# Optimization experiments

Hardware: AMD Instinct MI355X
Metric: run time of the kernel (lower is better)

## Reference

```python
import jax, jax.numpy as jnp
import numpy as np

B, T, HID = 2, 2048, 1024
NH = 8
QK_DIM = 1024
V_DIM = 2048
SCALE_BASE = 512.0
GN_EPS = 1e-5


def _xpos_rotate(x, downscale):
    # x: [B, T, QK_DIM]; XPOS rotary embedding (syncdoth/RetNet, offset=0)
    d = QK_DIM
    dh = d // 2
    pos = jnp.arange(T, dtype=jnp.float32)
    # per-pair magnitude scale
    base_scale = (jnp.arange(0, d, 2, dtype=jnp.float32) + 0.4 * d) / (1.4 * d)  # [dh]
    scale = base_scale[None, :] ** (pos[:, None] / SCALE_BASE)  # [T, dh]
    if downscale:
        scale = 1.0 / scale
    inv_freq = 1.0 / (10000.0 ** (jnp.arange(dh, dtype=jnp.float32) / dh))
    sinusoid = pos[:, None] * inv_freq[None, :]  # [T, dh]
    sin = jnp.sin(sinusoid) * scale
    cos = jnp.cos(sinusoid) * scale
    # duplicate_interleave -> [T, d]
    sin = jnp.repeat(sin, 2, axis=-1)
    cos = jnp.repeat(cos, 2, axis=-1)
    x1 = x[..., 0::2]
    x2 = x[..., 1::2]
    rot = jnp.stack((-x2, x1), axis=-1).reshape(x.shape)  # rotate_every_two
    return x * cos[None] + rot * sin[None]


def setup_inputs() -> dict:
    key = jax.random.key(0)
    k1, k2, k3, k4 = jax.random.split(key, 4)
    x = jax.random.normal(k1, (B, T, HID), dtype=jnp.float32)
    Wqkv = jax.random.normal(k2, (HID, 2 * QK_DIM + V_DIM), dtype=jnp.float32) / np.sqrt(HID)
    Wg = jax.random.normal(k3, (HID, V_DIM), dtype=jnp.float32) / np.sqrt(HID)
    Wp = jax.random.normal(k4, (V_DIM, HID), dtype=jnp.float32) / np.sqrt(V_DIM)
    bp = jnp.zeros((HID,), dtype=jnp.float32)
    return {"x": x, "Wqkv": Wqkv, "Wg": Wg, "Wp": Wp, "bp": bp}


def reference(x, Wqkv, Wg, Wp, bp):
    # multi-scale decay (non-default gamma path)
    gamma = 1.0 - jnp.exp(jnp.linspace(np.log(1.0 / 32), np.log(1.0 / 512), NH)).astype(jnp.float32)  # [NH]

    qkv = x @ Wqkv  # [B,T,2qk+v]
    q, k, v = jnp.split(qkv, [QK_DIM, 2 * QK_DIM], axis=-1)
    q = _xpos_rotate(q, downscale=False)
    k = _xpos_rotate(k, downscale=True)

    dqk = QK_DIM // NH
    dv = V_DIM // NH
    q = q.reshape(B, T, NH, dqk).transpose(0, 2, 1, 3)  # [B,H,T,dqk]
    k = k.reshape(B, T, NH, dqk).transpose(0, 2, 1, 3)
    v = v.reshape(B, T, NH, dv).transpose(0, 2, 1, 3)   # [B,H,T,dv]

    # parallel decay mask: gamma^(i-j) for i>=j else 0  -> [H,T,T]
    idx = jnp.arange(T)
    expo = idx[:, None] - idx[None, :]
    expo_safe = jnp.where(expo >= 0, expo, 0).astype(jnp.float32)
    decay_mask = jnp.where(expo[None] >= 0, gamma[:, None, None] ** expo_safe[None], 0.0)  # [H,T,T]

    scores = jnp.einsum('bhid,bhjd->bhij', q, k) * (dqk ** -0.5)
    retention = jnp.einsum('bhij,bhjv->bhiv', scores * decay_mask[None], v)  # [B,H,T,dv]

    # current_kv state: sum_t decay_mask[h,-1,t] * k_t (outer) v_t  -> [B,H,dqk,dv]
    curr_kv = jnp.einsum('bhtk,bhtv,ht->bhkv', k, v, decay_mask[:, -1, :])

    ret = retention.transpose(0, 2, 1, 3).reshape(B, T, V_DIM)

    # GroupNorm(num_groups=NH, affine=False) over [B*T, V_DIM]
    g = ret.reshape(B, T, NH, dv)
    mu = jnp.mean(g, axis=-1, keepdims=True)
    var = jnp.var(g, axis=-1, keepdims=True)
    normed = ((g - mu) / jnp.sqrt(var + GN_EPS)).reshape(B, T, V_DIM)

    gate = jax.nn.silu(x @ Wg)
    out = (gate * normed) @ Wp + bp
    return out, curr_kv
```

## Files before the change

kernel.cpp:

```cpp
#include <hip/hip_runtime.h>

typedef unsigned short u16;
typedef unsigned int   u32;
typedef unsigned long long u64;

typedef __attribute__((ext_vector_type(8))) short bf8_t;
typedef __attribute__((ext_vector_type(4))) float f4_t;

#define DEVI __device__ __forceinline__
#define MFMA16(a,b,c) __builtin_amdgcn_mfma_f32_16x16x32_bf16((a),(b),(c),0,0,0)

#define BB   2
#define TT   2048
#define HIDN 1024
#define L0f  (-3.4657359027997265f)
#define DLf  (-0.3960841031714215f)
#define SCL  (0.08838834764831845f)

DEVI u16 f2b(float f) {
    u32 u = __float_as_uint(f);
    u += 0x7FFFu + ((u >> 16) & 1u);
    return (u16)(u >> 16);
}
DEVI float b2f(u16 u) { return __uint_as_float(((u32)u) << 16); }

DEVI void gll16(const void* g, void* l) {
    __builtin_amdgcn_global_load_lds((const __attribute__((address_space(1))) void*)g,
                                     (__attribute__((address_space(3))) void*)l, 16, 0, 0);
}

DEVI void st_u16(u16* SM, int row, int col, u16 v) {
    *(u16*)((char*)SM + row * 256 + ((col * 2) ^ ((row & 15) << 4))) = v;
}
DEVI void cpout_u16(const u16* SM, u16* g, size_t rowStrB, int tid) {
#pragma unroll
    for (int it = 0; it < 8; it++) {
        int chunk = it * 256 + tid;
        int r = chunk >> 4, j = chunk & 15;
        uint4 v = *(const uint4*)((const char*)SM + r * 256 + ((j * 16) ^ ((r & 15) << 4)));
        *(uint4*)((char*)g + (size_t)r * rowStrB + j * 16) = v;
    }
}

__global__ __launch_bounds__(256) void k_tables(u32* __restrict__ cqp, u32* __restrict__ ckp) {
    int idx = blockIdx.x * 256 + threadIdx.x;
    int t = idx >> 9, m = idx & 511;
    float base = (2.f * (float)m + 409.6f) * (1.f / 1433.6f);
    float s = exp2f(log2f(base) * ((float)t * (1.f / 512.f)));
    float invf = exp2f(-(float)m * (13.287712379549449f / 512.f));
    float sn, cs;
    sincosf((float)t * invf, &sn, &cs);
    int h = m >> 6;
    float lg2h = log2f(1.f - expf(L0f + (float)h * DLf));
    float qf = s * SCL * exp2f((float)(t & 63) * lg2h);
    cqp[idx] = (u32)f2b(cs * qf) | ((u32)f2b(sn * qf) << 16);
    float is = 1.f / s;
    ckp[idx] = (u32)f2b(cs * is) | ((u32)f2b(sn * is) << 16);
}

__global__ __launch_bounds__(256) void k_gpow(float* __restrict__ gt, float* __restrict__ gk) {
    if (blockIdx.x == 64) {
#pragma unroll
        for (int s = 0; s < 2; s++) {
            int idx = threadIdx.x + s * 256;
            int h = idx >> 6, d = idx & 63;
            float lg2 = log2f(1.f - expf(L0f + (float)h * DLf));
            gk[idx] = exp2f(-(float)d * lg2);
        }
        return;
    }
    int i = blockIdx.x * 256 + threadIdx.x;
    int h = i >> 11, t = i & 2047;
    float lg2 = log2f(1.f - expf(L0f + (float)h * DLf));
    gt[i] = exp2f((float)(2047 - t) * lg2);
}

__global__ __launch_bounds__(256) void k_cvt(const float* __restrict__ in, u16* __restrict__ out) {
    int i = blockIdx.x * 256 + threadIdx.x;
    float4 v = ((const float4*)in)[i];
    u64 pk = (u64)f2b(v.x) | ((u64)f2b(v.y) << 16) | ((u64)f2b(v.z) << 32) | ((u64)f2b(v.w) << 48);
    ((u64*)out)[i] = pk;
}

__global__ __launch_bounds__(256) void k_tpose(const float* __restrict__ in, u16* __restrict__ out,
                                               int R, int C) {
    __shared__ float tile[32][33];
    int c0 = blockIdx.x * 32, r0 = blockIdx.y * 32;
    int tx = threadIdx.x, ty = threadIdx.y;
#pragma unroll
    for (int i = 0; i < 4; i++)
        tile[ty * 4 + i][tx] = in[(size_t)(r0 + ty * 4 + i) * C + c0 + tx];
    __syncthreads();
#pragma unroll
    for (int i = 0; i < 4; i++)
        out[(size_t)(c0 + ty * 4 + i) * R + r0 + tx] = f2b(tile[tx][ty * 4 + i]);
}

DEVI void gemm_ml(const u16* __restrict__ Ag, const u16* __restrict__ Bg, int Klen, int Kstr,
                  int m0, int n0, u16* As, u16* Bs, f4_t acc[4][4]) {
    int tid = threadIdx.x, lane = tid & 63, wid = tid >> 6;
    int wr = wid >> 1, wc = wid & 1, lr = lane & 15, lg = lane >> 4;
    for (int k0 = 0; k0 < Klen; k0 += 64) {
        __syncthreads();
#pragma unroll
        for (int p = 0; p < 4; p++) {
            int flat = p * 4096 + tid * 16;
            int row = flat >> 7, byt = (flat & 127) ^ ((row & 7) << 4);
            gll16((const char*)Ag + ((size_t)(m0 + row) * Kstr + k0) * 2 + byt,
                  (char*)As + p * 4096 + wid * 1024);
            gll16((const char*)Bg + ((size_t)(n0 + row) * Kstr + k0) * 2 + byt,
                  (char*)Bs + p * 4096 + wid * 1024);
        }
        __syncthreads();
#pragma unroll
        for (int kk = 0; kk < 2; kk++) {
            bf8_t a[4], b[4];
#pragma unroll
            for (int f = 0; f < 4; f++) {
                int ra = wr * 64 + f * 16 + lr;
                a[f] = *(const bf8_t*)((const char*)As + ra * 128 + ((kk * 64 + lg * 16) ^ ((ra & 7) << 4)));
                int rb = wc * 64 + f * 16 + lr;
                b[f] = *(const bf8_t*)((const char*)Bs + rb * 128 + ((kk * 64 + lg * 16) ^ ((rb & 7) << 4)));
            }
#pragma unroll
            for (int i = 0; i < 4; i++)
#pragma unroll
                for (int j = 0; j < 4; j++)
                    acc[i][j] = MFMA16(a[i], b[j], acc[i][j]);
        }
    }
}

DEVI void acc_zero(f4_t acc[4][4]) {
#pragma unroll
    for (int i = 0; i < 4; i++)
#pragma unroll
        for (int j = 0; j < 4; j++)
#pragma unroll
            for (int e = 0; e < 4; e++) acc[i][j][e] = 0.f;
}

__global__ __launch_bounds__(256) void k_gemm_qkvg(
    const u16* __restrict__ xb, const u16* __restrict__ Wcat,
    const u32* __restrict__ cqp, const u32* __restrict__ ckp, const float* __restrict__ gk,
    u16* __restrict__ qw, u16* __restrict__ kw, u16* __restrict__ kT, u16* __restrict__ vT,
    u16* __restrict__ gateb) {
    __shared__ u16 SM[128 * 128];
    f4_t acc[4][4]; acc_zero(acc);
    int m0 = blockIdx.y * 128, n0 = blockIdx.x * 128;
    gemm_ml(xb, Wcat, 1024, 1024, m0, n0, SM, SM + 128 * 64, acc);
    int tid = threadIdx.x, lane = tid & 63, wid = tid >> 6;
    int wr = wid >> 1, wc = wid & 1, lr = lane & 15, lg = lane >> 4;
    int b = m0 >> 11, t0 = m0 & 2047;
    __syncthreads();
    if (n0 < 2048) {
        int isK = n0 >= 1024;
        const u32* cT = isK ? ckp : cqp;
        int h = (n0 >> 7) & 7;
#pragma unroll
        for (int fm = 0; fm < 4; fm++)
#pragma unroll
            for (int fn = 0; fn < 4; fn++) {
                int col = wc * 64 + fn * 16 + lr;
                int mi = ((n0 & 1023) + col) >> 1;
                u64 pk = 0;
#pragma unroll
                for (int r = 0; r < 4; r++) {
                    int row = wr * 64 + fm * 16 + lg * 4 + r;
                    int t = t0 + row;
                    float v = acc[fm][fn][r];
                    float pv = __shfl_xor(v, 1);
                    u32 cp = cT[t * 512 + mi];
                    float cs = b2f((u16)cp), sn = b2f((u16)(cp >> 16));
                    float o = (col & 1) ? (v * cs + pv * sn) : (v * cs - pv * sn);
                    if (isK) {
                        pk |= ((u64)f2b(o)) << (16 * r);
                        o *= gk[h * 64 + (t & 63)];
                    }
                    st_u16(SM, row, col, f2b(o));
                }
                if (isK)
                    *(u64*)&kT[((size_t)((b * 8 + h) * 128 + col)) * 2048 + t0 + wr * 64 + fm * 16 + lg * 4] = pk;
            }
        __syncthreads();
        u16* g = (isK ? kw : qw) + ((size_t)((b * 8 + h) * 2048 + t0)) * 128;
        cpout_u16(SM, g, 256, tid);
    } else if (n0 < 4096) {
        int c0 = n0 - 2048, h = c0 >> 8, dv0 = c0 & 255;
#pragma unroll
        for (int fm = 0; fm < 4; fm++)
#pragma unroll
            for (int fn = 0; fn < 4; fn++) {
                int dv = wc * 64 + fn * 16 + lr;
                int tb = wr * 64 + fm * 16 + lg * 4;
                u64 pk = 0;
#pragma unroll
                for (int r = 0; r < 4; r++) pk |= ((u64)f2b(acc[fm][fn][r])) << (16 * r);
                *(u64*)((char*)SM + dv * 256 + ((tb * 2) ^ ((dv & 15) << 4))) = pk;
            }
        __syncthreads();
        u16* g = vT + ((size_t)((b * 8 + h) * 256 + dv0)) * 2048 + t0;
        cpout_u16(SM, g, 4096, tid);
    } else {
        int c0 = n0 - 4096;
#pragma unroll
        for (int fm = 0; fm < 4; fm++)
#pragma unroll
            for (int fn = 0; fn < 4; fn++) {
                int col = wc * 64 + fn * 16 + lr;
#pragma unroll
                for (int r = 0; r < 4; r++) {
                    int row = wr * 64 + fm * 16 + lg * 4 + r;
                    float gg = acc[fm][fn][r];
                    st_u16(SM, row, col, f2b(gg / (1.f + expf(-gg))));
                }
            }
        __syncthreads();
        u16* g = gateb + (size_t)(b * 2048 + t0) * 2048 + c0;
        cpout_u16(SM, g, 4096, tid);
    }
}

__global__ __launch_bounds__(256) void k_gemm_outp(const u16* __restrict__ gdb, const u16* __restrict__ Wt,
                                                   float* __restrict__ part) {
    __shared__ u16 SM[128 * 128];
    f4_t acc[4][4]; acc_zero(acc);
    int m0 = blockIdx.y * 128, n0 = blockIdx.x * 128, kz = blockIdx.z;
    gemm_ml(gdb + kz * 1024, Wt + kz * 1024, 1024, 2048, m0, n0, SM, SM + 128 * 64, acc);
    int tid = threadIdx.x, lane = tid & 63, wid = tid >> 6;
    int wr = wid >> 1, wc = wid & 1, lr = lane & 15, lg = lane >> 4;
    float* SMf = (float*)SM;
    float* po = part + (size_t)kz * 4096 * 1024;
    __syncthreads();
#pragma unroll
    for (int p = 0; p < 2; p++) {
        if (p) __syncthreads();
        if (wr == p) {
#pragma unroll
            for (int fm = 0; fm < 4; fm++)
#pragma unroll
                for (int fn = 0; fn < 4; fn++) {
                    int col = wc * 64 + fn * 16 + lr;
#pragma unroll
                    for (int r = 0; r < 4; r++) {
                        int rowl = fm * 16 + lg * 4 + r;
                        *(float*)((char*)SMf + rowl * 512 + ((col * 4) ^ ((rowl & 7) << 6))) = acc[fm][fn][r];
                    }
                }
        }
        __syncthreads();
#pragma unroll
        for (int it2 = 0; it2 < 8; it2++) {
            int chunk = it2 * 256 + tid;
            int rowl = chunk >> 5, j = chunk & 31;
            f4_t v = *(const f4_t*)((const char*)SMf + rowl * 512 + ((j * 16) ^ ((rowl & 7) << 6)));
            *(f4_t*)((char*)po + ((size_t)(m0 + p * 64 + rowl) * 1024 + n0) * 4 + j * 16) = v;
        }
    }
}

__global__ __launch_bounds__(256) void k_outred(const float* __restrict__ part, const float* __restrict__ bp,
                                                float* __restrict__ outp) {
    int i = blockIdx.x * 256 + threadIdx.x;
    f4_t a = ((const f4_t*)part)[i];
    f4_t c = ((const f4_t*)(part + (size_t)4096 * 1024))[i];
    f4_t bb = *(const f4_t*)(bp + ((i * 4) & 1023));
#pragma unroll
    for (int e = 0; e < 4; e++) a[e] += c[e] + bb[e];
    ((f4_t*)outp)[i] = a;
}

__global__ __launch_bounds__(256, 3) void k_retention(const u16* __restrict__ qws, const u16* __restrict__ kws,
                                                      const u16* __restrict__ vTws,
                                                      u16* __restrict__ ret0, u16* __restrict__ ret1) {
    __shared__ u16 SMr[64 * 128 + 256 * 64];
    u16* Ks = SMr;
    u16* Vs = SMr + 64 * 128;
    int x = blockIdx.x;
    int it, jlo, jhi, toret1;
    if (x < 16)      { it = 15 - x;  jlo = 0;              jhi = it + 1;         toret1 = 0; }
    else if (x < 32) { it = x;       jlo = 0;              jhi = (it + 2) >> 1;  toret1 = 0; }
    else             { it = x - 16;  jlo = (it + 2) >> 1;  jhi = it + 1;         toret1 = 1; }
    int h = blockIdx.y, b = blockIdx.z;
    int bh = b * 8 + h;
    float lg2 = log2f(1.f - expf(L0f + (float)h * DLf));
    int i0 = it * 64;
    const u16* qbase = qws + (size_t)bh * 2048 * 128;
    const u16* kbase = kws + (size_t)bh * 2048 * 128;
    const u16* vbase = vTws + (size_t)bh * 256 * 2048;
    int tid = threadIdx.x, lane = tid & 63, w = tid >> 6, lr = lane & 15, lg = lane >> 4;
    bf8_t aq[4];
#pragma unroll
    for (int kk = 0; kk < 4; kk++)
        aq[kk] = *(const bf8_t*)((const char*)qbase + (size_t)(i0 + w * 16 + lr) * 256 + kk * 64 + lg * 16);
    f4_t racc[16];
#pragma unroll
    for (int f = 0; f < 16; f++)
#pragma unroll
        for (int e = 0; e < 4; e++) racc[f][e] = 0.f;
    for (int jt = jlo; jt < jhi; jt++) {
        int j0 = jt * 64;
        int diag = (jt == it);
        float tf = exp2f(64.f * (float)(it - jt) * lg2);
        __syncthreads();
#pragma unroll
        for (int p = 0; p < 4; p++) {
            int flat = p * 4096 + tid * 16;
            int row = flat >> 8, byt = (flat & 255) ^ ((row & 7) << 4);
            gll16((const char*)kbase + (size_t)(j0 + row) * 256 + byt, (char*)Ks + p * 4096 + w * 1024);
        }
#pragma unroll
        for (int p = 0; p < 8; p++) {
            int flat = p * 4096 + tid * 16;
            int row = flat >> 7, byt = (flat & 127) ^ ((row & 7) << 4);
            gll16((const char*)vbase + (size_t)row * 4096 + (size_t)j0 * 2 + byt,
                  (char*)Vs + p * 4096 + w * 1024);
        }
        __syncthreads();
        f4_t sacc[4];
#pragma unroll
        for (int f = 0; f < 4; f++)
#pragma unroll
            for (int e = 0; e < 4; e++) sacc[f][e] = 0.f;
#pragma unroll
        for (int kk = 0; kk < 4; kk++)
#pragma unroll
            for (int fn = 0; fn < 4; fn++) {
                int rb = fn * 16 + lr;
                bf8_t bb = *(const bf8_t*)((const char*)Ks + rb * 256 + ((kk * 64 + lg * 16) ^ ((rb & 7) << 4)));
                sacc[fn] = MFMA16(aq[kk], bb, sacc[fn]);
            }
        __syncthreads();
#pragma unroll
        for (int fn = 0; fn < 4; fn++)
#pragma unroll
            for (int r = 0; r < 4; r++) {
                int i_loc = w * 16 + lg * 4 + r;
                int col = fn * 16 + lr;
                float v = diag ? ((i_loc - col >= 0) ? sacc[fn][r] : 0.f) : sacc[fn][r] * tf;
                *(u16*)((char*)Ks + i_loc * 128 + ((col * 2) ^ ((i_loc & 7) << 4))) = f2b(v);
            }
#pragma unroll
        for (int kk = 0; kk < 2; kk++) {
            int ra = w * 16 + lr;
            bf8_t ap = *(const bf8_t*)((const char*)Ks + ra * 128 + ((kk * 64 + lg * 16) ^ ((ra & 7) << 4)));
#pragma unroll
            for (int fn2 = 0; fn2 < 16; fn2++) {
                int rb = fn2 * 16 + lr;
                bf8_t bv = *(const bf8_t*)((const char*)Vs + rb * 128 + ((kk * 64 + lg * 16) ^ ((rb & 7) << 4)));
                racc[fn2] = MFMA16(ap, bv, racc[fn2]);
            }
        }
    }
    __syncthreads();
    u16* St = Vs;
#pragma unroll
    for (int fn2 = 0; fn2 < 16; fn2++)
#pragma unroll
        for (int r = 0; r < 4; r++) {
            int il = w * 16 + lg * 4 + r;
            int dv = fn2 * 16 + lr;
            *(u16*)((char*)St + il * 512 + ((dv * 2) ^ ((il & 15) << 4))) = f2b(racc[fn2][r]);
        }
    __syncthreads();
#pragma unroll
    for (int it2 = 0; it2 < 8; it2++) {
        int chunk = it2 * 256 + tid;
        int il = chunk >> 5, j = chunk & 31;
        uint4 v = *(const uint4*)((const char*)St + il * 512 + ((j * 16) ^ ((il & 15) << 4)));
        char* dst;
        if (toret1) dst = (char*)ret1 + ((size_t)(b * 1024 + i0 - 1024 + il) * 2048 + h * 256) * 2 + j * 16;
        else        dst = (char*)ret0 + ((size_t)(b * 2048 + i0 + il) * 2048 + h * 256) * 2 + j * 16;
        *(uint4*)dst = v;
    }
}

__global__ __launch_bounds__(512) void k_currkv(const u16* __restrict__ kTws, const u16* __restrict__ vTws,
                                                const float* __restrict__ gtab, float* __restrict__ part) {
    __shared__ u16 Ks2[128 * 64];
    __shared__ u16 Vws[256 * 64];
    int tr = blockIdx.x;
    int bh = blockIdx.y;
    int h = bh & 7;
    const u16* kT = kTws + (size_t)bh * 128 * 2048;
    const u16* vT = vTws + (size_t)bh * 256 * 2048;
    const float* gt = gtab + h * 2048;
    int tid = threadIdx.x, lane = tid & 63, wid = tid >> 6;
    int wr = wid >> 2, wc = wid & 3, lr = lane & 15, lg = lane >> 4;
    f4_t acc[4][4]; acc_zero(acc);
    for (int tc = 0; tc < 8; tc++) {
        int t0 = tr * 512 + tc * 64;
        __syncthreads();
#pragma unroll
        for (int p = 0; p < 2; p++) {
            int flat = p * 8192 + tid * 16;
            int row = flat >> 7, byt = (flat & 127) ^ ((row & 7) << 4);
            gll16((const char*)kT + (size_t)row * 4096 + (size_t)t0 * 2 + byt,
                  (char*)Ks2 + p * 8192 + wid * 1024);
        }
#pragma unroll
        for (int p = 0; p < 4; p++) {
            int flat = p * 8192 + tid * 16;
            int row = flat >> 7, byt = flat & 127;
            int tt = t0 + (byt >> 1);
            const u16* src = vT + (size_t)row * 2048 + tt;
            u16 tmp[8]; *(uint4*)tmp = *(const uint4*)src;
            const float* gp = gt + tt;
            u16 op[8];
#pragma unroll
            for (int e = 0; e < 8; e++) op[e] = f2b(b2f(tmp[e]) * gp[e]);
            *(uint4*)((char*)Vws + row * 128 + (byt ^ ((row & 7) << 4))) = *(uint4*)op;
        }
        __syncthreads();
#pragma unroll
        for (int kk = 0; kk < 2; kk++) {
            bf8_t a[4], bb[4];
#pragma unroll
            for (int f = 0; f < 4; f++) {
                int ra = wr * 64 + f * 16 + lr;
                a[f] = *(const bf8_t*)((const char*)Ks2 + ra * 128 + ((kk * 64 + lg * 16) ^ ((ra & 7) << 4)));
                int rb = wc * 64 + f * 16 + lr;
                bb[f] = *(const bf8_t*)((const char*)Vws + rb * 128 + ((kk * 64 + lg * 16) ^ ((rb & 7) << 4)));
            }
#pragma unroll
            for (int i = 0; i < 4; i++)
#pragma unroll
                for (int j = 0; j < 4; j++)
                    acc[i][j] = MFMA16(a[i], bb[j], acc[i][j]);
        }
    }
#pragma unroll
    for (int fm = 0; fm < 4; fm++)
#pragma unroll
        for (int fn = 0; fn < 4; fn++)
#pragma unroll
            for (int r = 0; r < 4; r++) {
                int dk = wr * 64 + fm * 16 + lg * 4 + r;
                int dv = wc * 64 + fn * 16 + lr;
                part[((size_t)(bh * 4 + tr)) * 32768 + (size_t)dk * 256 + dv] = acc[fm][fn][r];
            }
}

__global__ __launch_bounds__(256) void k_reduce_ckv(const float* __restrict__ part, float* __restrict__ outc) {
    int i = blockIdx.x * 256 + threadIdx.x;
    int bh = i >> 15, wv = i & 32767;
    float s = 0.f;
#pragma unroll
    for (int tr = 0; tr < 4; tr++) s += part[((size_t)(bh * 4 + tr)) * 32768 + wv];
    outc[i] = s;
}

__global__ __launch_bounds__(256) void k_gnorm(const u16* __restrict__ ret0, const u16* __restrict__ ret1,
                                               const u16* __restrict__ gateb, u16* __restrict__ gatedb) {
    int g = blockIdx.x * 4 + (threadIdx.x >> 6);
    int lane = threadIdx.x & 63;
    int row = g >> 3, h = g & 7;
    size_t base = (size_t)row * 2048 + h * 256 + lane * 4;
    u64 p0 = *(const u64*)(ret0 + base);
    float e0 = b2f((u16)p0), e1 = b2f((u16)(p0 >> 16)), e2 = b2f((u16)(p0 >> 32)), e3 = b2f((u16)(p0 >> 48));
    if ((row & 2047) >= 1024) {
        size_t b1 = (size_t)((row >> 11) * 1024 + (row & 1023)) * 2048 + h * 256 + lane * 4;
        u64 p1 = *(const u64*)(ret1 + b1);
        e0 += b2f((u16)p1); e1 += b2f((u16)(p1 >> 16)); e2 += b2f((u16)(p1 >> 32)); e3 += b2f((u16)(p1 >> 48));
    }
    float s = e0 + e1 + e2 + e3;
    float sqs = e0 * e0 + e1 * e1 + e2 * e2 + e3 * e3;
#pragma unroll
    for (int m = 1; m < 64; m <<= 1) { s += __shfl_xor(s, m); sqs += __shfl_xor(sqs, m); }
    float mean = s * (1.f / 256.f);
    float var = sqs * (1.f / 256.f) - mean * mean;
    float inv = rsqrtf(var + 1e-5f);
    u64 gp = *(const u64*)(gateb + base);
    u64 pk = (u64)f2b((e0 - mean) * inv * b2f((u16)gp)) |
             ((u64)f2b((e1 - mean) * inv * b2f((u16)(gp >> 16))) << 16) |
             ((u64)f2b((e2 - mean) * inv * b2f((u16)(gp >> 32))) << 32) |
             ((u64)f2b((e3 - mean) * inv * b2f((u16)(gp >> 48))) << 48);
    *(u64*)(gatedb + base) = pk;
}

extern "C" void kernel_launch(void* const* d_in, const int* in_sizes, int n_in,
                              void* d_out, int out_size, void* d_ws, size_t ws_size,
                              hipStream_t stream) {
    const float* x    = (const float*)d_in[0];
    const float* Wqkv = (const float*)d_in[1];
    const float* Wg   = (const float*)d_in[2];
    const float* Wp   = (const float*)d_in[3];
    const float* bp   = (const float*)d_in[4];
    float* outp   = (float*)d_out;
    float* outckv = outp + (size_t)BB * TT * HIDN;

    char* ws = (char*)d_ws;
    const size_t MB = 1024 * 1024;
    u16*   xb     = (u16*)(ws);
    u16*   WqkvT  = (u16*)(ws + 8 * MB);
    u16*   WgT    = (u16*)(ws + 16 * MB);
    u16*   WpT    = (u16*)(ws + 20 * MB);
    u32*   cqp    = (u32*)(ws + 24 * MB);
    u32*   ckp    = (u32*)(ws + 28 * MB);
    u16*   gateb  = (u16*)(ws + 32 * MB);
    u16*   qw     = (u16*)(ws + 48 * MB);
    u16*   kw     = (u16*)(ws + 56 * MB);
    u16*   kT     = (u16*)(ws + 64 * MB);
    u16*   vT     = (u16*)(ws + 72 * MB);
    u16*   ret0b  = (u16*)(ws + 88 * MB);
    u16*   ret1b  = (u16*)(ws + 104 * MB);
    float* ckvp   = (float*)(ws + 112 * MB);
    float* gtab   = (float*)(ws + 120 * MB);
    float* gkt    = (float*)(ws + 120 * MB + 65536);
    u16*   gatedb = (u16*)(ws + 48 * MB);
    float* opart  = (float*)(ws + 88 * MB);

    hipLaunchKernelGGL(k_tables, dim3(4096), dim3(256), 0, stream, cqp, ckp);
    hipLaunchKernelGGL(k_gpow, dim3(65), dim3(256), 0, stream, gtab, gkt);
    hipLaunchKernelGGL(k_cvt, dim3(4096), dim3(256), 0, stream, x, xb);
    hipLaunchKernelGGL(k_tpose, dim3(128, 32), dim3(32, 8), 0, stream, Wqkv, WqkvT, 1024, 4096);
    hipLaunchKernelGGL(k_tpose, dim3(64, 32),  dim3(32, 8), 0, stream, Wg,   WgT,   1024, 2048);
    hipLaunchKernelGGL(k_tpose, dim3(32, 64),  dim3(32, 8), 0, stream, Wp,   WpT,   2048, 1024);
    hipLaunchKernelGGL(k_gemm_qkvg, dim3(48, 32), dim3(256), 0, stream,
                       xb, WqkvT, cqp, ckp, gkt, qw, kw, kT, vT, gateb);
    hipLaunchKernelGGL(k_currkv, dim3(4, 16), dim3(512), 0, stream, kT, vT, gtab, ckvp);
    hipLaunchKernelGGL(k_reduce_ckv, dim3(2048), dim3(256), 0, stream, ckvp, outckv);
    hipLaunchKernelGGL(k_retention, dim3(48, 8, 2), dim3(256), 0, stream, qw, kw, vT, ret0b, ret1b);
    hipLaunchKernelGGL(k_gnorm, dim3(8192), dim3(256), 0, stream, ret0b, ret1b, gateb, gatedb);
    hipLaunchKernelGGL(k_gemm_outp, dim3(8, 32, 2), dim3(256), 0, stream, gatedb, WpT, opart);
    hipLaunchKernelGGL(k_outred, dim3(4096), dim3(256), 0, stream, opart, bp, outp);
}
```

Baseline: 251.3 us.

## Replace QKV/gate GEMM with 256x256 tile, double-buffered 8-wave kernel

Rewrites the fused QKV+gate projection GEMM to use 256x256 output tiles computed by 512 threads (8 waves). K-tiles of 64 are double-buffered in 128KB of LDS via async global-to-LDS loads. MFMA phases are interleaved with s_barrier and s_setprio, and blocks are remapped with a swizzle for L2 locality. Larger tiles raise data reuse and overlap loads with compute, at the cost of fewer blocks (384) and heavy LDS and register use.

```diff
diff --git a/kernel.cpp b/kernel.cpp
--- a/kernel.cpp
+++ b/kernel.cpp
@@ -27,19 +27,6 @@
 DEVI void gll16(const void* g, void* l) {
     __builtin_amdgcn_global_load_lds((const __attribute__((address_space(1))) void*)g,
                                      (__attribute__((address_space(3))) void*)l, 16, 0, 0);
-}
-
-DEVI void st_u16(u16* SM, int row, int col, u16 v) {
-    *(u16*)((char*)SM + row * 256 + ((col * 2) ^ ((row & 15) << 4))) = v;
-}
-DEVI void cpout_u16(const u16* SM, u16* g, size_t rowStrB, int tid) {
-#pragma unroll
-    for (int it = 0; it < 8; it++) {
-        int chunk = it * 256 + tid;
-        int r = chunk >> 4, j = chunk & 15;
-        uint4 v = *(const uint4*)((const char*)SM + r * 256 + ((j * 16) ^ ((r & 15) << 4)));
-        *(uint4*)((char*)g + (size_t)r * rowStrB + j * 16) = v;
-    }
 }
 
 __global__ __launch_bounds__(256) void k_tables(u32* __restrict__ cqp, u32* __restrict__ ckp) {
@@ -96,6 +83,164 @@
         out[(size_t)(c0 + ty * 4 + i) * R + r0 + tx] = f2b(tile[tx][ty * 4 + i]);
 }
 
+DEVI void stage_tile(const u16* __restrict__ A, const u16* __restrict__ B,
+                     int m0, int n0, int kt, char* buf, int tid, int wid) {
+#pragma unroll
+    for (int q = 0; q < 4; q++) {
+        int flat = q * 8192 + tid * 16;
+        int row = flat >> 7, byt = (flat & 127) ^ ((row & 7) << 4);
+        gll16((const char*)A + (size_t)(m0 + row) * 2048 + kt * 128 + byt,
+              buf + q * 8192 + wid * 1024);
+        gll16((const char*)B + (size_t)(n0 + row) * 2048 + kt * 128 + byt,
+              buf + 32768 + q * 8192 + wid * 1024);
+    }
+}
+
+#define QPHASE(kk, fmh, LOADB)                                                        \
+    {                                                                                 \
+        bf8_t a_[4];                                                                  \
+        _Pragma("unroll")                                                             \
+        for (int f = 0; f < 4; f++) {                                                 \
+            int ra = 128 * wr + ((fmh) * 4 + f) * 16 + lr;                            \
+            a_[f] = *(const bf8_t*)(bA + ra * 128 + (((kk) * 64 + lg * 16) ^ ((ra & 7) << 4))); \
+        }                                                                             \
+        if (LOADB) {                                                                  \
+            _Pragma("unroll")                                                         \
+            for (int f = 0; f < 4; f++) {                                             \
+                int rb = 64 * wc + f * 16 + lr;                                       \
+                breg[f] = *(const bf8_t*)(bB + rb * 128 + (((kk) * 64 + lg * 16) ^ ((rb & 7) << 4))); \
+            }                                                                         \
+        }                                                                             \
+        __builtin_amdgcn_s_barrier();                                                 \
+        __builtin_amdgcn_s_setprio(1);                                                \
+        _Pragma("unroll")                                                             \
+        for (int f = 0; f < 4; f++)                                                   \
+            _Pragma("unroll")                                                         \
+            for (int j = 0; j < 4; j++)                                               \
+                acc[(fmh) * 4 + f][j] = MFMA16(a_[f], breg[j], acc[(fmh) * 4 + f][j]); \
+        __builtin_amdgcn_s_setprio(0);                                                \
+        __builtin_amdgcn_s_barrier();                                                 \
+    }
+
+__global__ __launch_bounds__(512, 2) void k_gemm_qkvg8(
+    const u16* __restrict__ xb, const u16* __restrict__ Wcat,
+    const u32* __restrict__ cqp, const u32* __restrict__ ckp, const float* __restrict__ gkt,
+    u16* __restrict__ qw, u16* __restrict__ kw, u16* __restrict__ kT, u16* __restrict__ vT,
+    u16* __restrict__ gateb) {
+    __shared__ __align__(16) char L[131072];
+    int flat = blockIdx.x;
+    int swz = (flat & 7) * 48 + (flat >> 3);
+    int m0 = (swz / 24) * 256, n0 = (swz % 24) * 256;
+    int tid = threadIdx.x, lane = tid & 63, wid = tid >> 6;
+    int wr = wid >> 2, wc = wid & 3, lr = lane & 15, lg = lane >> 4;
+    f4_t acc[8][4];
+#pragma unroll
+    for (int i = 0; i < 8; i++)
+#pragma unroll
+        for (int j = 0; j < 4; j++)
+#pragma unroll
+            for (int e = 0; e < 4; e++) acc[i][j][e] = 0.f;
+    stage_tile(xb, Wcat, m0, n0, 0, L, tid, wid);
+    __syncthreads();
+    for (int kt = 0; kt < 16; ++kt) {
+        const char* bA = L + (kt & 1) * 65536;
+        const char* bB = bA + 32768;
+        if (kt < 15) stage_tile(xb, Wcat, m0, n0, kt + 1, L + ((kt + 1) & 1) * 65536, tid, wid);
+        bf8_t breg[4];
+        QPHASE(0, 0, 1)
+        QPHASE(0, 1, 0)
+        QPHASE(1, 0, 1)
+        QPHASE(1, 1, 0)
+        __syncthreads();
+    }
+    char* SP = L;
+    int b = m0 >> 11, t0 = m0 & 2047;
+    if (n0 < 4096 && n0 >= 2048) {
+        int h = (n0 - 2048) >> 8;
+#pragma unroll
+        for (int fm = 0; fm < 8; fm++)
+#pragma unroll
+            for (int fn = 0; fn < 4; fn++) {
+                int dv = wc * 64 + fn * 16 + lr;
+                int rowb = wr * 128 + fm * 16 + lg * 4;
+                u64 pk = 0;
+#pragma unroll
+                for (int r = 0; r < 4; r++) pk |= ((u64)f2b(acc[fm][fn][r])) << (16 * r);
+                *(u64*)(SP + dv * 512 + ((rowb * 2) ^ ((dv & 15) << 4))) = pk;
+            }
+        __syncthreads();
+#pragma unroll
+        for (int it = 0; it < 16; it++) {
+            int chunk = it * 512 + tid;
+            int dv = chunk >> 5, j = chunk & 31;
+            uint4 v = *(const uint4*)(SP + dv * 512 + ((j * 16) ^ ((dv & 15) << 4)));
+            *(uint4*)(vT + ((size_t)((b * 8 + h) * 256 + dv)) * 2048 + t0 + j * 8) = v;
+        }
+    } else if (n0 < 2048) {
+        int isK = n0 >= 1024;
+        const u32* cT = isK ? ckp : cqp;
+        int hb = (n0 >> 7) & 7;
+#pragma unroll
+        for (int fm = 0; fm < 8; fm++)
+#pragma unroll
+            for (int fn = 0; fn < 4; fn++) {
+                int col = wc * 64 + fn * 16 + lr;
+                int gq = (n0 & 1023) + col;
+                int mi = gq >> 1, h = gq >> 7;
+                u64 pk = 0;
+#pragma unroll
+                for (int r = 0; r < 4; r++) {
+                    int rowl = wr * 128 + fm * 16 + lg * 4 + r;
+                    int t = t0 + rowl;
+                    float v = acc[fm][fn][r];
+                    float pv = __shfl_xor(v, 1);
+                    u32 cp = cT[t * 512 + mi];
+                    float cs = b2f((u16)cp), sn = b2f((u16)(cp >> 16));
+                    float o = (col & 1) ? (v * cs + pv * sn) : (v * cs - pv * sn);
+                    if (isK) {
+                        pk |= ((u64)f2b(o)) << (16 * r);
+                        o *= gkt[h * 64 + (t & 63)];
+                    }
+                    *(u16*)(SP + rowl * 512 + ((col * 2) ^ ((rowl & 15) << 4))) = f2b(o);
+                }
+                if (isK)
+                    *(u64*)&kT[((size_t)((b * 8 + h) * 128 + (gq & 127))) * 2048 + t0 + wr * 128 + fm * 16 + lg * 4] = pk;
+            }
+        __syncthreads();
+#pragma unroll
+        for (int it = 0; it < 16; it++) {
+            int chunk = it * 512 + tid;
+            int r = chunk >> 5, j = chunk & 31;
+            uint4 v = *(const uint4*)(SP + r * 512 + ((j * 16) ^ ((r & 15) << 4)));
+            int hh = hb + (j >> 4);
+            u16* g = (isK ? kw : qw) + ((size_t)((b * 8 + hh) * 2048 + t0 + r)) * 128 + (j & 15) * 8;
+            *(uint4*)g = v;
+        }
+    } else {
+        int c0 = n0 - 4096;
+#pragma unroll
+        for (int fm = 0; fm < 8; fm++)
+#pragma unroll
+            for (int fn = 0; fn < 4; fn++) {
+                int col = wc * 64 + fn * 16 + lr;
+#pragma unroll
+                for (int r = 0; r < 4; r++) {
+                    int rowl = wr * 128 + fm * 16 + lg * 4 + r;
+                    float gg = acc[fm][fn][r];
+                    *(u16*)(SP + rowl * 512 + ((col * 2) ^ ((rowl & 15) << 4))) = f2b(gg / (1.f + expf(-gg)));
+                }
+            }
+        __syncthreads();
+#pragma unroll
+        for (int it = 0; it < 16; it++) {
+            int chunk = it * 512 + tid;
+            int r = chunk >> 5, j = chunk & 31;
+            uint4 v = *(const uint4*)(SP + r * 512 + ((j * 16) ^ ((r & 15) << 4)));
+            *(uint4*)(gateb + (size_t)(b * 2048 + t0 + r) * 2048 + c0 + j * 8) = v;
+        }
+    }
+}
+
 DEVI void gemm_ml(const u16* __restrict__ Ag, const u16* __restrict__ Bg, int Klen, int Kstr,
                   int m0, int n0, u16* As, u16* Bs, f4_t acc[4][4]) {
     int tid = threadIdx.x, lane = tid & 63, wid = tid >> 6;
@@ -138,87 +283,6 @@
         for (int j = 0; j < 4; j++)
 #pragma unroll
             for (int e = 0; e < 4; e++) acc[i][j][e] = 0.f;
-}
-
-__global__ __launch_bounds__(256) void k_gemm_qkvg(
-    const u16* __restrict__ xb, const u16* __restrict__ Wcat,
-    const u32* __restrict__ cqp, const u32* __restrict__ ckp, const float* __restrict__ gk,
-    u16* __restrict__ qw, u16* __restrict__ kw, u16* __restrict__ kT, u16* __restrict__ vT,
-    u16* __restrict__ gateb) {
-    __shared__ u16 SM[128 * 128];
-    f4_t acc[4][4]; acc_zero(acc);
-    int m0 = blockIdx.y * 128, n0 = blockIdx.x * 128;
-    gemm_ml(xb, Wcat, 1024, 1024, m0, n0, SM, SM + 128 * 64, acc);
-    int tid = threadIdx.x, lane = tid & 63, wid = tid >> 6;
-    int wr = wid >> 1, wc = wid & 1, lr = lane & 15, lg = lane >> 4;
-    int b = m0 >> 11, t0 = m0 & 2047;
-    __syncthreads();
-    if (n0 < 2048) {
-        int isK = n0 >= 1024;
-        const u32* cT = isK ? ckp : cqp;
-        int h = (n0 >> 7) & 7;
-#pragma unroll
-        for (int fm = 0; fm < 4; fm++)
-#pragma unroll
-            for (int fn = 0; fn < 4; fn++) {
-                int col = wc * 64 + fn * 16 + lr;
-                int mi = ((n0 & 1023) + col) >> 1;
-                u64 pk = 0;
-#pragma unroll
-                for (int r = 0; r < 4; r++) {
-                    int row = wr * 64 + fm * 16 + lg * 4 + r;
-                    int t = t0 + row;
-                    float v = acc[fm][fn][r];
-                    float pv = __shfl_xor(v, 1);
-                    u32 cp = cT[t * 512 + mi];
-                    float cs = b2f((u16)cp), sn = b2f((u16)(cp >> 16));
-                    float o = (col & 1) ? (v * cs + pv * sn) : (v * cs - pv * sn);
-                    if (isK) {
-                        pk |= ((u64)f2b(o)) << (16 * r);
-                        o *= gk[h * 64 + (t & 63)];
-                    }
-                    st_u16(SM, row, col, f2b(o));
-                }
-                if (isK)
-                    *(u64*)&kT[((size_t)((b * 8 + h) * 128 + col)) * 2048 + t0 + wr * 64 + fm * 16 + lg * 4] = pk;
-            }
-        __syncthreads();
-        u16* g = (isK ? kw : qw) + ((size_t)((b * 8 + h) * 2048 + t0)) * 128;
-        cpout_u16(SM, g, 256, tid);
-    } else if (n0 < 4096) {
-        int c0 = n0 - 2048, h = c0 >> 8, dv0 = c0 & 255;
-#pragma unroll
-        for (int fm = 0; fm < 4; fm++)
-#pragma unroll
-            for (int fn = 0; fn < 4; fn++) {
-                int dv = wc * 64 + fn * 16 + lr;
-                int tb = wr * 64 + fm * 16 + lg * 4;
-                u64 pk = 0;
-#pragma unroll
-                for (int r = 0; r < 4; r++) pk |= ((u64)f2b(acc[fm][fn][r])) << (16 * r);
-                *(u64*)((char*)SM + dv * 256 + ((tb * 2) ^ ((dv & 15) << 4))) = pk;
-            }
-        __syncthreads();
-        u16* g = vT + ((size_t)((b * 8 + h) * 256 + dv0)) * 2048 + t0;
-        cpout_u16(SM, g, 4096, tid);
-    } else {
-        int c0 = n0 - 4096;
-#pragma unroll
-        for (int fm = 0; fm < 4; fm++)
-#pragma unroll
-            for (int fn = 0; fn < 4; fn++) {
-                int col = wc * 64 + fn * 16 + lr;
-#pragma unroll
-                for (int r = 0; r < 4; r++) {
-                    int row = wr * 64 + fm * 16 + lg * 4 + r;
-                    float gg = acc[fm][fn][r];
-                    st_u16(SM, row, col, f2b(gg / (1.f + expf(-gg))));
-                }
-            }
-        __syncthreads();
-        u16* g = gateb + (size_t)(b * 2048 + t0) * 2048 + c0;
-        cpout_u16(SM, g, 4096, tid);
-    }
 }
 
 __global__ __launch_bounds__(256) void k_gemm_outp(const u16* __restrict__ gdb, const u16* __restrict__ Wt,
@@ -516,7 +580,7 @@
     hipLaunchKernelGGL(k_tpose, dim3(128, 32), dim3(32, 8), 0, stream, Wqkv, WqkvT, 1024, 4096);
     hipLaunchKernelGGL(k_tpose, dim3(64, 32),  dim3(32, 8), 0, stream, Wg,   WgT,   1024, 2048);
     hipLaunchKernelGGL(k_tpose, dim3(32, 64),  dim3(32, 8), 0, stream, Wp,   WpT,   2048, 1024);
-    hipLaunchKernelGGL(k_gemm_qkvg, dim3(48, 32), dim3(256), 0, stream,
+    hipLaunchKernelGGL(k_gemm_qkvg8, dim3(384), dim3(512), 0, stream,
                        xb, WqkvT, cqp, ckp, gkt, qw, kw, kT, vT, gateb);
     hipLaunchKernelGGL(k_currkv, dim3(4, 16), dim3(512), 0, stream, kT, vT, gtab, ckvp);
     hipLaunchKernelGGL(k_reduce_ckv, dim3(2048), dim3(256), 0, stream, ckvp, outckv);
```

Measured after the change: 231.3 us. 1.09x faster.
